# Performance work log

Hardware: AMD Instinct MI355X
Metric: run time of the kernel (lower is better)

## Reference

```python
import jax, jax.numpy as jnp
import numpy as np

D_MODEL = 64  # per-head dim; temper = sqrt(D_MODEL)
NEG_INF = -1e30  # stand-in for -inf; safe under softmax and autodiff


def setup_inputs() -> dict:
    key = jax.random.key(0)
    kq, kk, kv, km = jax.random.split(key, 4)
    B, S, D = 16, 2048, 64
    q = jax.random.normal(kq, (B, S, D), dtype=jnp.float32)
    k = jax.random.normal(kk, (B, S, D), dtype=jnp.float32)
    v = jax.random.normal(kv, (B, S, D), dtype=jnp.float32)
    attn_mask = jax.random.bernoulli(km, 0.1, (B, S, S))
    return {"q": q, "k": k, "v": v, "attn_mask": attn_mask}


def reference(q, k, v, attn_mask):
    temper = jnp.sqrt(jnp.float32(D_MODEL))
    # [B, Sq, Sk] scores
    attn = jnp.einsum("bqd,bkd->bqk", q, k) / temper
    attn = jnp.where(attn_mask, NEG_INF, attn)
    attn = jax.nn.softmax(attn, axis=2)
    # dropout is identity in eval / attn_dropout=0.0
    output = jnp.einsum("bqk,bkd->bqd", attn, v)
    return (output, attn)
```

## Files before the change

### kernel.cpp

```cpp
#include <hip/hip_runtime.h>
#include <hip/hip_bf16.h>
#include <stdint.h>


#define S_DIM 2048
#define D_DIM 64

typedef short short8 __attribute__((ext_vector_type(8)));
typedef float floatx4 __attribute__((ext_vector_type(4)));
typedef unsigned short ushort8v __attribute__((ext_vector_type(8)));
typedef uint32_t u32a __attribute__((may_alias));

__device__ __forceinline__ unsigned short f2bf(float x) {
    uint32_t u = __float_as_uint(x);
    u += 0x7fffu + ((u >> 16) & 1u);
    return (unsigned short)(u >> 16);
}
__device__ __forceinline__ float bf2f(unsigned short h) {
    return __uint_as_float((uint32_t)h << 16);
}

__global__ __launch_bounds__(256) void prep_mask(
    const int* __restrict__ mask, uint32_t* __restrict__ bits)
{
    size_t i = (size_t)blockIdx.x * 256 + threadIdx.x;
    int m = mask[i];
    unsigned long long bal = __ballot(m != 0);
    int lane = threadIdx.x & 63;
    if ((lane & 31) == 0)
        bits[i >> 5] = (uint32_t)(bal >> ((lane >> 5) * 32));
}

__global__ __launch_bounds__(128) void prep_k2(
    const float* __restrict__ k,
    unsigned short* __restrict__ khi2, unsigned short* __restrict__ klo2)
{
    const int b  = blockIdx.x >> 7;
    const int kc = blockIdx.x & 127;
    const int t  = threadIdx.x;
    const int s = t >> 6, quad = (t >> 4) & 3, n16 = t & 15;
    const float* src = k + ((size_t)(b * S_DIM) + kc * 16 + n16) * D_DIM + s * 32 + quad * 8;
    float4 x0 = *(const float4*)src;
    float4 x1 = *(const float4*)(src + 4);
    float xs[8] = {x0.x, x0.y, x0.z, x0.w, x1.x, x1.y, x1.z, x1.w};
    ushort8v h, l;
    #pragma unroll
    for (int e = 0; e < 8; ++e) {
        unsigned short hp = f2bf(xs[e]);
        h[e] = hp;
        l[e] = f2bf(xs[e] - bf2f(hp));
    }
    size_t o = ((size_t)(b * 128 + kc)) * 1024 + (size_t)t * 8;
    *(ushort8v*)(khi2 + o) = h;
    *(ushort8v*)(klo2 + o) = l;
}

__global__ __launch_bounds__(256) void prep_v2(
    const float* __restrict__ v, unsigned short* __restrict__ vfrag)
{
    const int b  = blockIdx.x >> 6;
    const int kb = blockIdx.x & 63;
    const int t  = threadIdx.x;
    const int nc = t >> 6, quad = (t >> 4) & 3, n16 = t & 15;
    ushort8v o;
    #pragma unroll
    for (int e = 0; e < 8; ++e) {
        float x = v[((size_t)(b * S_DIM) + kb * 32 + quad * 8 + e) * D_DIM + nc * 16 + n16];
        o[e] = f2bf(x);
    }
    *(ushort8v*)(vfrag + ((size_t)(b * 64 + kb)) * 2048 + (size_t)t * 8) = o;
}

__global__ __launch_bounds__(512) void attn_fused_v3(
    const float* __restrict__ q,
    const unsigned short* __restrict__ khi2, const unsigned short* __restrict__ klo2,
    const unsigned short* __restrict__ vfrag,
    const uint32_t* __restrict__ bits,
    float* __restrict__ out, float* __restrict__ attn)
{
    __shared__ __align__(16) float qlds[16 * 68];
    __shared__ __align__(16) unsigned short pbuf[8 * 16 * 36];
    __shared__ __align__(16) float obuf[8 * 16 * 68];
    __shared__ float mxtab[8 * 16];
    __shared__ float ltab[8 * 16];

    const int tid  = threadIdx.x;
    const int w    = tid >> 6;
    const int lane = tid & 63;
    const int quad = lane >> 4;
    const int n16  = lane & 15;
    const int b    = blockIdx.x >> 7;
    const int q0   = (blockIdx.x & 127) * 16;
    const int key0 = w * 256;

    uint32_t blo, bhi;
    {
        const uint32_t* bsrc = bits +
            ((size_t)(b * S_DIM) + q0 + (lane >> 2)) * 64 + w * 8 + 2 * (lane & 3);
        uint2 bt = *(const uint2*)bsrc;
        blo = bt.x; bhi = bt.y;
    }

    {
        int m = tid >> 5, d = (tid & 31) * 2;
        float2 qv = *(const float2*)(q + ((size_t)(b * S_DIM + q0 + m)) * D_DIM + d);
        qlds[m * 68 + d]     = qv.x;
        qlds[m * 68 + d + 1] = qv.y;
    }
    __syncthreads();

    short8 ahi[2], alo[2];
    #pragma unroll
    for (int s = 0; s < 2; ++s) {
        const float* qp = &qlds[n16 * 68 + s * 32 + quad * 8];
        union { unsigned short u[8]; short8 v; } H, L;
        #pragma unroll
        for (int p = 0; p < 8; ++p) {
            float x = qp[p];
            unsigned short hp = f2bf(x);
            H.u[p] = hp;
            L.u[p] = f2bf(x - bf2f(hp));
        }
        ahi[s] = H.v; alo[s] = L.v;
    }

    floatx4 sc[16];
    const unsigned short* khb = khi2 + (size_t)b * 131072;
    const unsigned short* klb = klo2 + (size_t)b * 131072;
    #pragma unroll
    for (int c = 0; c < 16; ++c) {
        const int kc = w * 16 + c;
        floatx4 acc = {0.f, 0.f, 0.f, 0.f};
        #pragma unroll
        for (int s = 0; s < 2; ++s) {
            const size_t off = (size_t)((kc * 2 + s) * 4 + quad) * 128 + n16 * 8;
            short8 BH = *(const short8*)(khb + off);
            short8 BL = *(const short8*)(klb + off);
            acc = __builtin_amdgcn_mfma_f32_16x16x32_bf16(ahi[s], BH, acc, 0, 0, 0);
            acc = __builtin_amdgcn_mfma_f32_16x16x32_bf16(ahi[s], BL, acc, 0, 0, 0);
            acc = __builtin_amdgcn_mfma_f32_16x16x32_bf16(alo[s], BH, acc, 0, 0, 0);
        }
        sc[c] = acc;
    }
    #pragma unroll
    for (int r = 0; r < 4; ++r) {
        #pragma unroll
        for (int c = 0; c < 16; ++c) {
            int srcl = quad * 16 + r * 4 + (c >> 2);
            uint32_t d = (uint32_t)__shfl((int)((c & 2) ? bhi : blo), srcl, 64);
            uint32_t bit = (d >> ((c & 1) * 16 + n16)) & 1u;
            sc[c][r] = bit ? -1e30f : sc[c][r] * 0.125f;
        }
    }

    #pragma unroll
    for (int r = 0; r < 4; ++r) {
        float mx = sc[0][r];
        #pragma unroll
        for (int c = 1; c < 16; ++c) mx = fmaxf(mx, sc[c][r]);
        #pragma unroll
        for (int o = 1; o < 16; o <<= 1) mx = fmaxf(mx, __shfl_xor(mx, o, 64));
        if (n16 == 0) mxtab[w * 16 + quad * 4 + r] = mx;
    }
    __syncthreads();
    #pragma unroll
    for (int r = 0; r < 4; ++r) {
        float mf = -3e38f;
        #pragma unroll
        for (int w2 = 0; w2 < 8; ++w2) mf = fmaxf(mf, mxtab[w2 * 16 + quad * 4 + r]);
        float l = 0.f;
        #pragma unroll
        for (int c = 0; c < 16; ++c) {
            float e = __expf(sc[c][r] - mf);
            sc[c][r] = e;
            l += e;
        }
        #pragma unroll
        for (int o = 1; o < 16; o <<= 1) l += __shfl_xor(l, o, 64);
        if (n16 == 0) ltab[w * 16 + quad * 4 + r] = l;
    }
    __syncthreads();
    #pragma unroll
    for (int r = 0; r < 4; ++r) {
        float l = 0.f;
        #pragma unroll
        for (int w2 = 0; w2 < 8; ++w2) l += ltab[w2 * 16 + quad * 4 + r];
        float inv = 1.0f / l;
        #pragma unroll
        for (int c = 0; c < 16; ++c) sc[c][r] *= inv;
    }

    {
        float* arow = attn + (size_t)(b * S_DIM + q0 + quad * 4) * S_DIM + key0 + n16;
        #pragma unroll
        for (int c = 0; c < 16; ++c) {
            #pragma unroll
            for (int r = 0; r < 4; ++r) arow[(size_t)r * S_DIM + c * 16] = sc[c][r];
        }
    }

    floatx4 o0 = {0,0,0,0}, o1 = {0,0,0,0}, o2 = {0,0,0,0}, o3 = {0,0,0,0};
    unsigned short* pw = pbuf + w * 576;
    const unsigned short* vtb = vfrag + (size_t)b * 131072;
    #pragma unroll
    for (int s2 = 0; s2 < 8; ++s2) {
        #pragma unroll
        for (int h = 0; h < 2; ++h) {
            const int c = s2 * 2 + h;
            #pragma unroll
            for (int r = 0; r < 4; ++r)
                pw[(quad * 4 + r) * 36 + h * 16 + n16] = f2bf(sc[c][r]);
        }
        short8 pa;
        {
            const u32a* pr = (const u32a*)((const char*)pbuf +
                                   (size_t)w * 1152 + n16 * 72 + quad * 16);
            union { uint32_t u[4]; short8 v; } P;
            P.u[0] = pr[0]; P.u[1] = pr[1]; P.u[2] = pr[2]; P.u[3] = pr[3];
            pa = P.v;
        }
        const int kb = w * 8 + s2;
        #pragma unroll
        for (int nc = 0; nc < 4; ++nc) {
            const size_t off = (size_t)((kb * 4 + nc) * 4 + quad) * 128 + n16 * 8;
            short8 bv = *(const short8*)(vtb + off);
            floatx4& oo = (nc == 0 ? o0 : nc == 1 ? o1 : nc == 2 ? o2 : o3);
            oo = __builtin_amdgcn_mfma_f32_16x16x32_bf16(pa, bv, oo, 0, 0, 0);
        }
    }

    #pragma unroll
    for (int nc = 0; nc < 4; ++nc) {
        floatx4 oo = (nc == 0 ? o0 : nc == 1 ? o1 : nc == 2 ? o2 : o3);
        #pragma unroll
        for (int i = 0; i < 4; ++i)
            obuf[(w * 16 + quad * 4 + i) * 68 + nc * 16 + n16] = oo[i];
    }
    __syncthreads();
    #pragma unroll
    for (int t2 = 0; t2 < 2; ++t2) {
        int idx = tid + t2 * 512;
        int m = idx >> 6, d = idx & 63;
        float a = 0.f;
        #pragma unroll
        for (int w2 = 0; w2 < 8; ++w2) a += obuf[(w2 * 16 + m) * 68 + d];
        out[(size_t)(b * S_DIM + q0 + m) * D_DIM + d] = a;
    }
}

__global__ __launch_bounds__(512) void attn_fused_v1(
    const float* __restrict__ q, const float* __restrict__ k,
    const float* __restrict__ v, const int* __restrict__ mask,
    float* __restrict__ out, float* __restrict__ attn)
{
    __shared__ __align__(16) float qlds[16 * 68];
    __shared__ __align__(16) unsigned short pbuf[8 * 16 * 36];
    __shared__ __align__(16) float obuf[8 * 16 * 68];
    __shared__ float mxtab[8 * 16];
    __shared__ float ltab[8 * 16];

    const int tid  = threadIdx.x;
    const int w    = tid >> 6;
    const int lane = tid & 63;
    const int quad = lane >> 4;
    const int n16  = lane & 15;
    const int b    = blockIdx.x >> 7;
    const int q0   = (blockIdx.x & 127) * 16;
    const int key0 = w * 256;

    {
        int m = tid >> 5, d = (tid & 31) * 2;
        float2 qv = *(const float2*)(q + ((size_t)(b * S_DIM + q0 + m)) * D_DIM + d);
        qlds[m * 68 + d]     = qv.x;
        qlds[m * 68 + d + 1] = qv.y;
    }
    __syncthreads();

    short8 ahi[2], alo[2];
    #pragma unroll
    for (int s = 0; s < 2; ++s) {
        const float* qp = &qlds[n16 * 68 + s * 32 + quad * 8];
        union { __hip_bfloat162 h[4]; short8 v; } H, L;
        #pragma unroll
        for (int p = 0; p < 4; ++p) {
            float x0 = qp[2 * p], x1 = qp[2 * p + 1];
            __hip_bfloat162 h2 = __float22bfloat162_rn(float2{x0, x1});
            float l0 = x0 - __bfloat162float(h2.x);
            float l1 = x1 - __bfloat162float(h2.y);
            H.h[p] = h2;
            L.h[p] = __float22bfloat162_rn(float2{l0, l1});
        }
        ahi[s] = H.v; alo[s] = L.v;
    }

    floatx4 sc[16];
    const size_t kvbase = (size_t)(b * S_DIM) * D_DIM;
    #pragma unroll
    for (int c = 0; c < 16; ++c) {
        const int key = key0 + c * 16 + n16;
        const int* mp = mask + (size_t)(b * S_DIM + q0 + quad * 4) * S_DIM + key;
        int mk0 = mp[0], mk1 = mp[S_DIM], mk2 = mp[2 * S_DIM], mk3 = mp[3 * S_DIM];
        floatx4 acc = {0.f, 0.f, 0.f, 0.f};
        #pragma unroll
        for (int s = 0; s < 2; ++s) {
            const float* kp = k + kvbase + (size_t)key * D_DIM + s * 32 + quad * 8;
            float4 k0 = *(const float4*)kp;
            float4 k1 = *(const float4*)(kp + 4);
            float kf[8] = {k0.x, k0.y, k0.z, k0.w, k1.x, k1.y, k1.z, k1.w};
            union { __hip_bfloat162 h[4]; short8 v; } BH, BL;
            #pragma unroll
            for (int p = 0; p < 4; ++p) {
                float x0 = kf[2 * p], x1 = kf[2 * p + 1];
                __hip_bfloat162 h2 = __float22bfloat162_rn(float2{x0, x1});
                BH.h[p] = h2;
                BL.h[p] = __float22bfloat162_rn(
                    float2{x0 - __bfloat162float(h2.x), x1 - __bfloat162float(h2.y)});
            }
            acc = __builtin_amdgcn_mfma_f32_16x16x32_bf16(ahi[s], BH.v, acc, 0, 0, 0);
            acc = __builtin_amdgcn_mfma_f32_16x16x32_bf16(ahi[s], BL.v, acc, 0, 0, 0);
            acc = __builtin_amdgcn_mfma_f32_16x16x32_bf16(alo[s], BH.v, acc, 0, 0, 0);
        }
        sc[c][0] = mk0 ? -1e30f : acc[0] * 0.125f;
        sc[c][1] = mk1 ? -1e30f : acc[1] * 0.125f;
        sc[c][2] = mk2 ? -1e30f : acc[2] * 0.125f;
        sc[c][3] = mk3 ? -1e30f : acc[3] * 0.125f;
    }

    #pragma unroll
    for (int r = 0; r < 4; ++r) {
        float mx = sc[0][r];
        #pragma unroll
        for (int c = 1; c < 16; ++c) mx = fmaxf(mx, sc[c][r]);
        #pragma unroll
        for (int o = 1; o < 16; o <<= 1) mx = fmaxf(mx, __shfl_xor(mx, o, 64));
        if (n16 == 0) mxtab[w * 16 + quad * 4 + r] = mx;
    }
    __syncthreads();
    #pragma unroll
    for (int r = 0; r < 4; ++r) {
        float mf = -3e38f;
        #pragma unroll
        for (int w2 = 0; w2 < 8; ++w2) mf = fmaxf(mf, mxtab[w2 * 16 + quad * 4 + r]);
        float l = 0.f;
        #pragma unroll
        for (int c = 0; c < 16; ++c) {
            float e = __expf(sc[c][r] - mf);
            sc[c][r] = e;
            l += e;
        }
        #pragma unroll
        for (int o = 1; o < 16; o <<= 1) l += __shfl_xor(l, o, 64);
        if (n16 == 0) ltab[w * 16 + quad * 4 + r] = l;
    }
    __syncthreads();
    #pragma unroll
    for (int r = 0; r < 4; ++r) {
        float l = 0.f;
        #pragma unroll
        for (int w2 = 0; w2 < 8; ++w2) l += ltab[w2 * 16 + quad * 4 + r];
        float inv = 1.0f / l;
        #pragma unroll
        for (int c = 0; c < 16; ++c) sc[c][r] *= inv;
    }

    {
        float* arow = attn + (size_t)(b * S_DIM + q0 + quad * 4) * S_DIM + key0 + n16;
        #pragma unroll
        for (int c = 0; c < 16; ++c) {
            #pragma unroll
            for (int r = 0; r < 4; ++r) arow[(size_t)r * S_DIM + c * 16] = sc[c][r];
        }
    }

    floatx4 o0 = {0,0,0,0}, o1 = {0,0,0,0}, o2 = {0,0,0,0}, o3 = {0,0,0,0};
    unsigned short* pw = pbuf + w * 576;
    #pragma unroll
    for (int s2 = 0; s2 < 8; ++s2) {
        #pragma unroll
        for (int h = 0; h < 2; ++h) {
            const int c = s2 * 2 + h;
            #pragma unroll
            for (int r = 0; r < 4; ++r)
                pw[(quad * 4 + r) * 36 + h * 16 + n16] = f2bf(sc[c][r]);
        }
        __syncthreads();
        short8 pa;
        {
            const uint32_t* pr = (const uint32_t*)((const char*)pbuf +
                                   (size_t)w * 1152 + n16 * 72 + quad * 16);
            union { uint32_t u[4]; short8 v; } P;
            P.u[0] = pr[0]; P.u[1] = pr[1]; P.u[2] = pr[2]; P.u[3] = pr[3];
            pa = P.v;
        }
        const size_t vrow0 = (size_t)(b * S_DIM + key0 + s2 * 32 + quad * 8) * D_DIM;
        #pragma unroll
        for (int nc = 0; nc < 4; ++nc) {
            const float* vp = v + vrow0 + nc * 16 + n16;
            union { __hip_bfloat162 h[4]; short8 v8; } BV;
            #pragma unroll
            for (int p = 0; p < 4; ++p) {
                float x0 = vp[(size_t)(2 * p) * D_DIM];
                float x1 = vp[(size_t)(2 * p + 1) * D_DIM];
                BV.h[p] = __float22bfloat162_rn(float2{x0, x1});
            }
            floatx4& oo = (nc == 0 ? o0 : nc == 1 ? o1 : nc == 2 ? o2 : o3);
            oo = __builtin_amdgcn_mfma_f32_16x16x32_bf16(pa, BV.v8, oo, 0, 0, 0);
        }
        __syncthreads();
    }

    #pragma unroll
    for (int nc = 0; nc < 4; ++nc) {
        floatx4 oo = (nc == 0 ? o0 : nc == 1 ? o1 : nc == 2 ? o2 : o3);
        #pragma unroll
        for (int i = 0; i < 4; ++i)
            obuf[(w * 16 + quad * 4 + i) * 68 + nc * 16 + n16] = oo[i];
    }
    __syncthreads();
    #pragma unroll
    for (int t2 = 0; t2 < 2; ++t2) {
        int idx = tid + t2 * 512;
        int m = idx >> 6, d = idx & 63;
        float a = 0.f;
        #pragma unroll
        for (int w2 = 0; w2 < 8; ++w2) a += obuf[(w2 * 16 + m) * 68 + d];
        out[(size_t)(b * S_DIM + q0 + m) * D_DIM + d] = a;
    }
}

extern "C" void kernel_launch(void* const* d_in, const int* in_sizes, int n_in,
                              void* d_out, int out_size, void* d_ws, size_t ws_size,
                              hipStream_t stream) {
    const float* q    = (const float*)d_in[0];
    const float* k    = (const float*)d_in[1];
    const float* v    = (const float*)d_in[2];
    const int*   mask = (const int*)d_in[3];

    float* out  = (float*)d_out;
    float* attn = out + (size_t)16 * S_DIM * D_DIM;

    const size_t NE = (size_t)16 * S_DIM * D_DIM;
    const size_t need = NE * 2 * 3 + NE * 4;
    if (d_ws != nullptr && ws_size >= need) {
        unsigned short* khi2  = (unsigned short*)d_ws;
        unsigned short* klo2  = khi2 + NE;
        unsigned short* vfrag = klo2 + NE;
        uint32_t*       bits  = (uint32_t*)(vfrag + NE);
        prep_mask<<<dim3(262144), dim3(256), 0, stream>>>(mask, bits);
        prep_k2<<<dim3(2048), dim3(128), 0, stream>>>(k, khi2, klo2);
        prep_v2<<<dim3(1024), dim3(256), 0, stream>>>(v, vfrag);
        attn_fused_v3<<<dim3(2048), dim3(512), 0, stream>>>(q, khi2, klo2, vfrag, bits, out, attn);
    } else {
        attn_fused_v1<<<dim3(2048), dim3(512), 0, stream>>>(q, k, v, mask, out, attn);
    }
}
```

Before: 634.8 us.

## Merge prep kernels into one launch and use nontemporal stores for attn

Folds the three preprocessing kernels (mask bit-packing, K hi/lo bf16 split, V fragment packing) into a single kernel that branches on block index, so two launches go away. The mask section now has each block handle 32 chunks instead of one, cutting the block count from 262144 to 8192. The large attn probability matrix is now written with nontemporal stores so it does not evict K/V data from cache. The cost is a heterogeneous kernel with divergent block roles, and nontemporal stores may change write coalescing behaviour.

New measurement: 580.2 us. 1.09x faster.

```diff
diff --git a/kernel.cpp b/kernel.cpp
--- a/kernel.cpp
+++ b/kernel.cpp
@@ -20,58 +20,64 @@
     return __uint_as_float((uint32_t)h << 16);
 }
 
-__global__ __launch_bounds__(256) void prep_mask(
-    const int* __restrict__ mask, uint32_t* __restrict__ bits)
-{
-    size_t i = (size_t)blockIdx.x * 256 + threadIdx.x;
-    int m = mask[i];
-    unsigned long long bal = __ballot(m != 0);
-    int lane = threadIdx.x & 63;
-    if ((lane & 31) == 0)
-        bits[i >> 5] = (uint32_t)(bal >> ((lane >> 5) * 32));
-}
-
-__global__ __launch_bounds__(128) void prep_k2(
+__global__ __launch_bounds__(256) void prep_all(
+    const int* __restrict__ mask, uint32_t* __restrict__ bits,
     const float* __restrict__ k,
-    unsigned short* __restrict__ khi2, unsigned short* __restrict__ klo2)
-{
-    const int b  = blockIdx.x >> 7;
-    const int kc = blockIdx.x & 127;
-    const int t  = threadIdx.x;
-    const int s = t >> 6, quad = (t >> 4) & 3, n16 = t & 15;
-    const float* src = k + ((size_t)(b * S_DIM) + kc * 16 + n16) * D_DIM + s * 32 + quad * 8;
-    float4 x0 = *(const float4*)src;
-    float4 x1 = *(const float4*)(src + 4);
-    float xs[8] = {x0.x, x0.y, x0.z, x0.w, x1.x, x1.y, x1.z, x1.w};
-    ushort8v h, l;
-    #pragma unroll
-    for (int e = 0; e < 8; ++e) {
-        unsigned short hp = f2bf(xs[e]);
-        h[e] = hp;
-        l[e] = f2bf(xs[e] - bf2f(hp));
-    }
-    size_t o = ((size_t)(b * 128 + kc)) * 1024 + (size_t)t * 8;
-    *(ushort8v*)(khi2 + o) = h;
-    *(ushort8v*)(klo2 + o) = l;
-}
-
-__global__ __launch_bounds__(256) void prep_v2(
+    unsigned short* __restrict__ khi2, unsigned short* __restrict__ klo2,
     const float* __restrict__ v, unsigned short* __restrict__ vfrag)
 {
-    const int b  = blockIdx.x >> 6;
-    const int kb = blockIdx.x & 63;
-    const int t  = threadIdx.x;
-    const int nc = t >> 6, quad = (t >> 4) & 3, n16 = t & 15;
-    ushort8v o;
-    #pragma unroll
-    for (int e = 0; e < 8; ++e) {
-        float x = v[((size_t)(b * S_DIM) + kb * 32 + quad * 8 + e) * D_DIM + nc * 16 + n16];
-        o[e] = f2bf(x);
-    }
-    *(ushort8v*)(vfrag + ((size_t)(b * 64 + kb)) * 2048 + (size_t)t * 8) = o;
-}
-
-__global__ __launch_bounds__(512) void attn_fused_v3(
+    const int blk = blockIdx.x;
+    const int tid = threadIdx.x;
+
+    if (blk < 8192) {
+        const size_t base = (size_t)blk * 8192;
+        const int lane = tid & 63;
+        const size_t wbase = base + (size_t)(tid & ~63);
+        #pragma unroll
+        for (int j = 0; j < 32; ++j) {
+            int m = mask[base + j * 256 + tid];
+            unsigned long long bal = __ballot(m != 0);
+            if ((lane & 31) == 0) {
+                size_t wb = wbase + j * 256;
+                bits[(wb >> 5) + (lane >> 5)] = (uint32_t)(bal >> ((lane >> 5) * 32));
+            }
+        }
+    } else if (blk < 9216) {
+        const int e  = blk - 8192;
+        const int b  = e >> 6;
+        const int kc = (e & 63) * 2 + (tid >> 7);
+        const int t  = tid & 127;
+        const int s = t >> 6, quad = (t >> 4) & 3, n16 = t & 15;
+        const float* src = k + ((size_t)(b * S_DIM) + kc * 16 + n16) * D_DIM + s * 32 + quad * 8;
+        float4 x0 = *(const float4*)src;
+        float4 x1 = *(const float4*)(src + 4);
+        float xs[8] = {x0.x, x0.y, x0.z, x0.w, x1.x, x1.y, x1.z, x1.w};
+        ushort8v h, l;
+        #pragma unroll
+        for (int p = 0; p < 8; ++p) {
+            unsigned short hp = f2bf(xs[p]);
+            h[p] = hp;
+            l[p] = f2bf(xs[p] - bf2f(hp));
+        }
+        size_t o = ((size_t)(b * 128 + kc)) * 1024 + (size_t)t * 8;
+        *(ushort8v*)(khi2 + o) = h;
+        *(ushort8v*)(klo2 + o) = l;
+    } else {
+        const int e  = blk - 9216;
+        const int b  = e >> 6;
+        const int kb = e & 63;
+        const int nc = tid >> 6, quad = (tid >> 4) & 3, n16 = tid & 15;
+        ushort8v o;
+        #pragma unroll
+        for (int p = 0; p < 8; ++p) {
+            float x = v[((size_t)(b * S_DIM) + kb * 32 + quad * 8 + p) * D_DIM + nc * 16 + n16];
+            o[p] = f2bf(x);
+        }
+        *(ushort8v*)(vfrag + ((size_t)(b * 64 + kb)) * 2048 + (size_t)tid * 8) = o;
+    }
+}
+
+__global__ __launch_bounds__(512) void attn_fused_v4(
     const float* __restrict__ q,
     const unsigned short* __restrict__ khi2, const unsigned short* __restrict__ klo2,
     const unsigned short* __restrict__ vfrag,
@@ -195,7 +201,8 @@
         #pragma unroll
         for (int c = 0; c < 16; ++c) {
             #pragma unroll
-            for (int r = 0; r < 4; ++r) arow[(size_t)r * S_DIM + c * 16] = sc[c][r];
+            for (int r = 0; r < 4; ++r)
+                __builtin_nontemporal_store(sc[c][r], arow + (size_t)r * S_DIM + c * 16);
         }
     }
 
@@ -446,10 +453,8 @@
         unsigned short* klo2  = khi2 + NE;
         unsigned short* vfrag = klo2 + NE;
         uint32_t*       bits  = (uint32_t*)(vfrag + NE);
-        prep_mask<<<dim3(262144), dim3(256), 0, stream>>>(mask, bits);
-        prep_k2<<<dim3(2048), dim3(128), 0, stream>>>(k, khi2, klo2);
-        prep_v2<<<dim3(1024), dim3(256), 0, stream>>>(v, vfrag);
-        attn_fused_v3<<<dim3(2048), dim3(512), 0, stream>>>(q, khi2, klo2, vfrag, bits, out, attn);
+        prep_all<<<dim3(10240), dim3(256), 0, stream>>>(mask, bits, k, khi2, klo2, v, vfrag);
+        attn_fused_v4<<<dim3(2048), dim3(512), 0, stream>>>(q, khi2, klo2, vfrag, bits, out, attn);
     } else {
         attn_fused_v1<<<dim3(2048), dim3(512), 0, stream>>>(q, k, v, mask, out, attn);
     }
```
